# Performance work log

Measured on AMD Instinct MI355X. Metric: run time of the kernel, lower is better.

The kernel has to match this reference:

```python
import jax, jax.numpy as jnp
from jax import lax
import numpy as np

B, C_IN, H, W = 4, 64, 192, 192
NPT = 128          # num_point
MAXC = 32          # objects per image
INIT_STRIDE, COARSE_STRIDE, DOWN = 10.0, 4.0, 4.0


def setup_inputs() -> dict:
    key = jax.random.key(0)
    ks = jax.random.split(key, 8)
    wh_pred = jax.random.normal(ks[0], (B, 2 * NPT, H, W), jnp.float32)
    cnn_feature = jax.random.normal(ks[1], (B, C_IN, H, W), jnp.float32)
    conv1_w = jax.random.normal(ks[2], (256, C_IN, 3, 3), jnp.float32) * 0.05
    conv1_b = jnp.zeros((256,), jnp.float32)
    conv2_w = jax.random.normal(ks[3], (C_IN, 256, 1, 1), jnp.float32) * 0.05
    conv2_b = jnp.zeros((C_IN,), jnp.float32)
    w_poly = jax.random.normal(ks[4], (NPT * 4, (NPT + 1) * C_IN), jnp.float32) * 0.02
    w_fuse = jax.random.normal(ks[5], (NPT * 2, NPT * 4), jnp.float32) * 0.02
    b_fuse = jnp.zeros((NPT * 2,), jnp.float32)
    ct_ind = jax.random.randint(ks[6], (B, MAXC), 0, H * W, jnp.int32)
    ct_img_idx = jnp.repeat(jnp.arange(B, dtype=jnp.int32), MAXC).reshape(B, MAXC)
    ct_num = jnp.full((B,), MAXC, jnp.int32)
    return {"wh_pred": wh_pred, "cnn_feature": cnn_feature,
            "conv1_w": conv1_w, "conv1_b": conv1_b, "conv2_w": conv2_w, "conv2_b": conv2_b,
            "w_poly": w_poly, "w_fuse": w_fuse, "b_fuse": b_fuse,
            "ct_ind": ct_ind, "ct_img_idx": ct_img_idx, "ct_num": ct_num}


def _conv(x, w, b, pad):
    y = lax.conv_general_dilated(x, w, (1, 1), [(pad, pad), (pad, pad)],
                                 dimension_numbers=("NCHW", "OIHW", "NCHW"))
    return y + b[None, :, None, None]


def _pnp(polys, h, w):
    # even-odd ray-casting rasterization: polys [N,P,2] (x,y) -> masks [N,h,w]
    N, P, _ = polys.shape
    yy = jnp.arange(h, dtype=polys.dtype)[None, :, None]   # [1,h,1]
    xx = jnp.arange(w, dtype=polys.dtype)[None, None, :]   # [1,1,w]
    v2 = jnp.roll(polys, -1, axis=1)
    edges = (polys[:, :, 0].T, polys[:, :, 1].T, v2[:, :, 0].T, v2[:, :, 1].T)  # each [P,N]

    def step(par, e):
        x1, y1, x2, y2 = [a[:, None, None] for a in e]      # [N,1,1]
        cond = (y1 > yy) != (y2 > yy)
        den = y2 - y1
        den = jnp.where(jnp.abs(den) < 1e-9, 1e-9, den)
        xint = x1 + (x2 - x1) * (yy - y1) / den
        return jnp.logical_xor(par, cond & (xx < xint)), None

    par0 = jnp.zeros((N, h, w), dtype=bool)
    par, _ = lax.scan(step, par0, edges)
    return par.astype(polys.dtype)


def _mask_batch(mask, ct_num, bs, h, w):
    # faithful to original buggy scatter: offset uses ct_num[i-1], not a cumulative sum
    cn = [int(v) for v in np.asarray(ct_num)]
    mc = max(cn)
    mb = jnp.zeros((bs, mc, h, w), mask.dtype)
    mb = mb.at[0, :cn[0]].set(mask[:cn[0]])
    for i in range(1, bs):
        mb = mb.at[i, :cn[i]].set(mask[cn[i - 1]:cn[i - 1] + cn[i]])
    return mb


def _sample(feat, pts, img_idx):
    # bilinear grid_sample (align_corners=False, zero padding): feat [B,C,H,W], pts [N,P,2] pixel coords
    Bf, C, Hf, Wf = feat.shape
    x = pts[..., 0] - 0.5
    y = pts[..., 1] - 0.5
    x0f = jnp.floor(x); y0f = jnp.floor(y)
    wx = (x - x0f)[..., None]; wy = (y - y0f)[..., None]
    x0 = x0f.astype(jnp.int32); y0 = y0f.astype(jnp.int32)

    def g(xi, yi):
        valid = (xi >= 0) & (xi < Wf) & (yi >= 0) & (yi < Hf)
        v = feat[img_idx[:, None], :, jnp.clip(yi, 0, Hf - 1), jnp.clip(xi, 0, Wf - 1)]  # [N,P,C]
        return v * valid[..., None]

    out = (g(x0, y0) * (1 - wx) * (1 - wy) + g(x0 + 1, y0) * wx * (1 - wy)
           + g(x0, y0 + 1) * (1 - wx) * wy + g(x0 + 1, y0 + 1) * wx * wy)
    return jnp.transpose(out, (0, 2, 1))  # [N,C,P]


def _decode(wh_pred, cnn_feature, conv1_w, conv1_b, conv2_w, conv2_b,
            w_poly, w_fuse, b_fuse, ct_ind, ct_img_idx, ct_num):
    bs, _, h, w = cnn_feature.shape
    ind = ct_ind.reshape(-1)        # ct_01 assumed all valid
    img = ct_img_idx.reshape(-1)
    cx = ind % w
    cy = ind // w
    off = wh_pred[img, :, cy, cx].reshape(ind.shape[0], -1, 2)   # [N, num_point, 2]
    ct = jnp.stack([cx, cy], axis=1).astype(wh_pred.dtype)       # [N,2]
    init_polys = off * INIT_STRIDE + ct[:, None, :]

    # Refine_wtih_pnp.trans_feature
    t = jax.nn.relu(_conv(cnn_feature, conv1_w, conv1_b, 1))
    feat = _conv(t, conv2_w, conv2_b, 0)

    # PnP_contour_feature (init)
    m_init = _pnp(init_polys, h, w)
    mb_init = _mask_batch(m_init, ct_num, bs, h, w)
    feat = jax.nn.relu(jnp.max(mb_init, axis=1, keepdims=True) * feat + feat)

    # GCN-style point feature sampling + global deform
    pts = jnp.concatenate([ct[:, None, :], init_polys], axis=1)  # [N, P+1, 2]
    fp = _sample(feat, pts, img).reshape(ind.shape[0], -1)       # [N, C*(P+1)]
    offsets = ((fp @ w_poly.T) @ w_fuse.T + b_fuse).reshape(-1, NPT, 2)
    coarse = offsets * COARSE_STRIDE + lax.stop_gradient(init_polys)

    # coarse_pnp
    m_c = _pnp(coarse, h, w)
    mb_c = _mask_batch(m_c, ct_num, bs, h, w)
    feat = jax.nn.relu(jnp.max(mb_c, axis=1, keepdims=True) * feat + feat)

    return init_polys * DOWN, coarse * DOWN, mb_init, mb_c, feat


def reference(wh_pred, cnn_feature, conv1_w, conv1_b, conv2_w, conv2_b,
              w_poly, w_fuse, b_fuse, ct_ind, ct_img_idx, ct_num):
    return _decode(wh_pred, cnn_feature, conv1_w, conv1_b, conv2_w, conv2_b,
                   w_poly, w_fuse, b_fuse, ct_ind, ct_img_idx, ct_num)
```

## Files before the change

### kernel.cpp

```cpp
#include <hip/hip_runtime.h>
#include <hip/hip_bf16.h>

#define HH 192
#define WW 192
#define HW 36864
#define CHW 2359296

typedef __attribute__((ext_vector_type(8))) short short8;
typedef __attribute__((ext_vector_type(4))) float float4v;

static __device__ __forceinline__ unsigned short f2bu(float f) {
  union { float f; unsigned u; } v; v.f = f;
  unsigned r = (v.u + 0x7fffu + ((v.u >> 16) & 1u)) >> 16;
  return (unsigned short)r;
}

static __device__ __forceinline__ float bu2f(unsigned short s) {
  union { unsigned u; float f; } v; v.u = ((unsigned)s) << 16;
  return v.f;
}

__global__ void k_prep(const float* __restrict__ c1w, const float* __restrict__ c2w,
                       const float* __restrict__ wfuse,
                       unsigned short* __restrict__ wB1, unsigned short* __restrict__ wB2,
                       float* __restrict__ wfT, float* __restrict__ tmp,
                       float* __restrict__ u01) {
  int i = blockIdx.x * 256 + threadIdx.x;
  if (i < 147456) {
    int T = i / 9216, r = i % 9216;
    int s = r / 512, e = r % 512;
    int l = e >> 3, j = e & 7;
    int m = l & 15, q = l >> 4;
    int oc = T * 16 + m;
    int k = s * 32 + q * 8 + j;
    int tap = k >> 6, ic = k & 63;
    int ky = tap / 3, kx = tap % 3;
    wB1[i] = f2bu(c1w[((oc * 64 + ic) * 3 + ky) * 3 + kx]);
    return;
  }
  int j2 = i - 147456;
  if (j2 < 16384) {
    int g = j2 / 512, e = j2 % 512;
    int l = e >> 3, jj = e & 7;
    int m = l & 15, q = l >> 4;
    int w = g / 8, s2 = g % 8;
    wB2[j2] = f2bu(c2w[(w * 16 + m) * 256 + s2 * 32 + q * 8 + jj]);
    return;
  }
  int k3 = j2 - 16384;
  if (k3 < 131072) { int jj = k3 >> 8, r = k3 & 255; wfT[k3] = wfuse[r * 512 + jj]; return; }
  int z = k3 - 131072;
  if (z < 65536) { tmp[z] = 0.f; return; }
  int v = z - 65536;
  if (v < 294912) u01[v] = 0.f;
}

__global__ void k_init_polys(const float* __restrict__ wh, const int* __restrict__ ct_ind,
                             const int* __restrict__ ct_img,
                             float* __restrict__ initp, float* __restrict__ out0) {
  int n = blockIdx.x;
  int p = threadIdx.x;
  int ind = ct_ind[n], img = ct_img[n];
  int cx = ind % WW, cy = ind / WW;
  size_t base = ((size_t)(img * 256 + 2 * p)) * HW + (size_t)cy * WW + cx;
  float ox = wh[base];
  float oy = wh[base + HW];
  float px = __fadd_rn(__fmul_rn(ox, 10.0f), (float)cx);
  float py = __fadd_rn(__fmul_rn(oy, 10.0f), (float)cy);
  initp[n * 256 + 2 * p]     = px;
  initp[n * 256 + 2 * p + 1] = py;
  out0[n * 256 + 2 * p]      = __fmul_rn(px, 4.0f);
  out0[n * 256 + 2 * p + 1]  = __fmul_rn(py, 4.0f);
}

__global__ __launch_bounds__(256, 3) void k_conv(const float* __restrict__ x,
    const unsigned short* __restrict__ wB1, const float* __restrict__ b1,
    const unsigned short* __restrict__ wB2, const float* __restrict__ b2,
    const float* __restrict__ u0, float* __restrict__ feat,
    unsigned short* __restrict__ featT) {
  int blk = blockIdx.x;
  int b    = blk / 576;
  int rem  = blk % 576;
  int pair = rem / 6;
  int xs   = rem % 6;
  int y0 = pair * 2, x0 = xs * 32;
  int t = threadIdx.x;
  int w = t >> 6, l = t & 63;
  int m = l & 15, q = l >> 4;

  __shared__ __align__(16) unsigned short sb[16896];

  {
    int kq = t & 7;
    int pr = t >> 3;
    for (int itr = 0; itr < 8; ++itr) {
      int pi = itr * 32 + pr;
      int r  = pi >> 6;
      int ic = pi & 63;
      int gy = y0 + r - 1;
      float4v v = (float4v){0.f, 0.f, 0.f, 0.f};
      if (gy >= 0 && gy < HH)
        v = *(const float4v*)&x[(size_t)(b * 64 + ic) * HW + (size_t)gy * WW + x0 + kq * 4];
      int base = (r * 34 + 1 + kq * 4) * 72 + ic;
      sb[base]       = f2bu(v[0]);
      sb[base + 72]  = f2bu(v[1]);
      sb[base + 144] = f2bu(v[2]);
      sb[base + 216] = f2bu(v[3]);
    }
    for (int itr = 0; itr < 2; ++itr) {
      int e = itr * 256 + t;
      int xxh = e >> 8;
      int rm = e & 255;
      int r = rm >> 6, ic = rm & 63;
      int gy = y0 + r - 1;
      int gx = x0 - 1 + xxh * 33;
      float v = 0.f;
      if (gy >= 0 && gy < HH && gx >= 0 && gx < WW)
        v = x[(size_t)(b * 64 + ic) * HW + (size_t)gy * WW + gx];
      sb[(r * 34 + xxh * 33) * 72 + ic] = f2bu(v);
    }
  }
  __syncthreads();

  float4v acc1[4][4];
#pragma unroll
  for (int nt = 0; nt < 4; ++nt) {
    float bv = b1[w * 64 + nt * 16 + m];
#pragma unroll
    for (int mt = 0; mt < 4; ++mt) acc1[mt][nt] = (float4v){bv, bv, bv, bv};
  }

#pragma unroll
  for (int s = 0; s < 18; ++s) {
    int tap = s >> 1, ky = tap / 3, kx = tap - ky * 3;
    int ic0 = (s & 1) * 32 + q * 8;
    short8 bF[4];
#pragma unroll
    for (int nt = 0; nt < 4; ++nt)
      bF[nt] = *(const short8*)&wB1[(size_t)((((w * 4 + nt) * 18 + s) * 512) + l * 8)];
    short8 aF[4];
#pragma unroll
    for (int mt = 0; mt < 4; ++mt) {
      int col  = (mt & 1) * 16 + m + kx;
      int rowi = ky + (mt >> 1);
      aF[mt] = *(const short8*)&sb[(rowi * 34 + col) * 72 + ic0];
    }
#pragma unroll
    for (int nt = 0; nt < 4; ++nt)
#pragma unroll
      for (int mt = 0; mt < 4; ++mt)
        acc1[mt][nt] = __builtin_amdgcn_mfma_f32_16x16x32_bf16(aF[mt], bF[nt], acc1[mt][nt], 0, 0, 0);
  }
  __syncthreads();

#pragma unroll
  for (int mt = 0; mt < 4; ++mt)
#pragma unroll
    for (int nt = 0; nt < 4; ++nt)
#pragma unroll
      for (int r = 0; r < 4; ++r) {
        int p = mt * 16 + q * 4 + r;
        int oc = w * 64 + nt * 16 + m;
        sb[p * 264 + oc] = f2bu(fmaxf(acc1[mt][nt][r], 0.f));
      }
  __syncthreads();

  float4v acc2[4];
  {
    float bv = b2[w * 16 + m];
#pragma unroll
    for (int mt = 0; mt < 4; ++mt) acc2[mt] = (float4v){bv, bv, bv, bv};
  }
#pragma unroll
  for (int s2 = 0; s2 < 8; ++s2) {
    short8 bF2 = *(const short8*)&wB2[(size_t)(((w * 8 + s2) * 512) + l * 8)];
#pragma unroll
    for (int mt = 0; mt < 4; ++mt) {
      short8 a2 = *(const short8*)&sb[(mt * 16 + m) * 264 + s2 * 32 + q * 8];
      acc2[mt] = __builtin_amdgcn_mfma_f32_16x16x32_bf16(a2, bF2, acc2[mt], 0, 0, 0);
    }
  }
  __syncthreads();

  float* fS = (float*)sb;
#pragma unroll
  for (int mt = 0; mt < 4; ++mt)
#pragma unroll
    for (int r = 0; r < 4; ++r) {
      int p = mt * 16 + q * 4 + r;
      fS[w * 1088 + m * 68 + p] = acc2[mt][r];
    }
  const float* ub = u0 + b * HW;
  {
    int gy = y0 + (l >> 5), gx = x0 + (l & 31);
    float uu = ub[gy * WW + gx];
    size_t fb = (size_t)(b * 64 + w * 16) * HW + (size_t)gy * WW + gx;
#pragma unroll
    for (int i = 0; i < 16; ++i) {
      float f = fS[w * 1088 + i * 68 + l];
      feat[fb + (size_t)i * HW] = fmaxf(uu * f + f, 0.f);
    }
  }
  {
    unsigned short* ft = featT + (size_t)b * HW * 64;
    int c2 = (l & 7) * 2;
#pragma unroll
    for (int i = 0; i < 8; ++i) {
      int p = (l >> 3) + 8 * i;
      float f0 = fS[w * 1088 + c2 * 68 + p];
      float f1 = fS[w * 1088 + (c2 + 1) * 68 + p];
      int gy = y0 + (p >> 5), gx = x0 + (p & 31);
      float uu = ub[gy * WW + gx];
      f0 = fmaxf(uu * f0 + f0, 0.f);
      f1 = fmaxf(uu * f1 + f1, 0.f);
      unsigned v = (unsigned)f2bu(f0) | ((unsigned)f2bu(f1) << 16);
      *(unsigned*)&ft[((size_t)(gy * WW + gx)) * 64 + w * 16 + c2] = v;
    }
  }
}

__global__ __launch_bounds__(64) void k_pnp(const float* __restrict__ polys,
                                            float* __restrict__ outm,
                                            float* __restrict__ u) {
  int row  = blockIdx.x;
  int n    = blockIdx.y;
  int lane = threadIdx.x;
  __shared__ float vx[128], vy[128], xint[128];
  __shared__ int cnt;
  if (lane == 0) cnt = 0;
  vx[lane]      = polys[n * 256 + 2 * lane];
  vy[lane]      = polys[n * 256 + 2 * lane + 1];
  vx[lane + 64] = polys[n * 256 + 2 * (lane + 64)];
  vy[lane + 64] = polys[n * 256 + 2 * (lane + 64) + 1];
  __syncthreads();
  float yy = (float)row;
  for (int e = lane; e < 128; e += 64) {
    float y1 = vy[e], y2 = vy[(e + 1) & 127];
    if ((y1 > yy) != (y2 > yy)) {
      float x1 = vx[e], x2 = vx[(e + 1) & 127];
      float den = __fsub_rn(y2, y1);
      if (fabsf(den) < 1e-9f) den = 1e-9f;
      float xi = __fadd_rn(x1, __fdiv_rn(__fmul_rn(__fsub_rn(x2, x1), __fsub_rn(yy, y1)), den));
      xint[atomicAdd(&cnt, 1)] = xi;
    }
  }
  __syncthreads();
  int mm = cnt;
  int bb = (n < 32) ? 0 : 1;
  int cc = n & 31;
  size_t base = ((size_t)(bb * 32 + cc) * HH + row) * WW;
  for (int xp = lane; xp < WW; xp += 64) {
    float xf = (float)xp;
    int c = 0;
    for (int j = 0; j < mm; ++j) c += (xf < xint[j]) ? 1 : 0;
    float mv = (float)(c & 1);
    outm[base + xp] = mv;
    if (n >= 32) {
      outm[base + (size_t)32 * HW + xp] = mv;
      outm[base + (size_t)64 * HW + xp] = mv;
    }
    if (c & 1) {
      int off = bb * HW + row * WW + xp;
      atomicOr((int*)(u + off), 0x3f800000);
      if (n >= 32) {
        atomicOr((int*)(u + off + HW), 0x3f800000);
        atomicOr((int*)(u + off + 2 * HW), 0x3f800000);
      }
    }
  }
}

__global__ __launch_bounds__(256) void k_sample(const unsigned short* __restrict__ featT,
    const float* __restrict__ initp, const int* __restrict__ ct_ind,
    const int* __restrict__ ct_img, float* __restrict__ fp) {
  int n  = blockIdx.x;
  int ch = blockIdx.y;
  int t  = threadIdx.x;
  int w  = t >> 6, lane = t & 63;
  int c  = lane & 31;
  int ph = lane >> 5;

  __shared__ float sF[4128];

  int img = ct_img[n];
  int ind = ct_ind[n];
  float ctx = (float)(ind % WW), cty = (float)(ind / WW);
  const unsigned short* fb = featT + (size_t)img * HW * 64 + ch * 32 + c;

  for (int i = 0; i < 17; ++i) {
    int p = i * 8 + w * 2 + ph;
    if (p < 129) {
      float px, py;
      if (p == 0) { px = ctx; py = cty; }
      else {
        px = initp[n * 256 + 2 * (p - 1)];
        py = initp[n * 256 + 2 * (p - 1) + 1];
      }
      float x = __fsub_rn(px, 0.5f), y = __fsub_rn(py, 0.5f);
      float x0f = floorf(x), y0f = floorf(y);
      float wx = __fsub_rn(x, x0f), wy = __fsub_rn(y, y0f);
      int x0 = (int)x0f, y0 = (int)y0f;
      float g[4];
#pragma unroll
      for (int qq = 0; qq < 4; ++qq) {
        int xi = x0 + (qq & 1), yi = y0 + (qq >> 1);
        bool valid = (xi >= 0) && (xi < WW) && (yi >= 0) && (yi < HH);
        int xc = min(max(xi, 0), WW - 1), yc = min(max(yi, 0), HH - 1);
        float v = bu2f(fb[(size_t)(yc * WW + xc) * 64]);
        g[qq] = valid ? v : 0.f;
      }
      float omx = __fsub_rn(1.f, wx), omy = __fsub_rn(1.f, wy);
      float r = __fadd_rn(__fadd_rn(__fadd_rn(
          __fmul_rn(__fmul_rn(g[0], omx), omy),
          __fmul_rn(__fmul_rn(g[1], wx),  omy)),
          __fmul_rn(__fmul_rn(g[2], omx), wy)),
          __fmul_rn(__fmul_rn(g[3], wx),  wy));
      sF[c * 129 + p] = r;
    }
  }
  __syncthreads();
  float* dst = fp + (size_t)n * 8256 + (size_t)ch * 4128;
  for (int idx = t; idx < 4128; idx += 256) dst[idx] = sF[idx];
}

__global__ __launch_bounds__(256) void k_gemm1(const float* __restrict__ fp,
    const float* __restrict__ wpoly, float* __restrict__ tmp) {
  int ntile = blockIdx.x;
  int jtile = blockIdx.y;
  int ks    = blockIdx.z;
  int c0 = (129 * ks) / 32, c1 = (129 * (ks + 1)) / 32;
  int t = threadIdx.x;
  int tn = t & 15, tj = t >> 4;
  __shared__ float aS[64][65];
  __shared__ float bS[64][65];
  float acc[4][4];
#pragma unroll
  for (int i = 0; i < 4; ++i)
#pragma unroll
    for (int j = 0; j < 4; ++j) acc[i][j] = 0.f;
  for (int ch = c0; ch < c1; ++ch) {
    int k0 = ch * 64;
    __syncthreads();
    for (int idx = t; idx < 4096; idx += 256) {
      int r = idx >> 6, cc = idx & 63;
      aS[cc][r] = fp[(size_t)(ntile * 64 + r) * 8256 + k0 + cc];
      bS[cc][r] = wpoly[(size_t)(jtile * 64 + r) * 8256 + k0 + cc];
    }
    __syncthreads();
    for (int kk = 0; kk < 64; ++kk) {
      float a0 = aS[kk][tn * 4], a1 = aS[kk][tn * 4 + 1], a2 = aS[kk][tn * 4 + 2], a3 = aS[kk][tn * 4 + 3];
      float b0 = bS[kk][tj * 4], b1 = bS[kk][tj * 4 + 1], b2 = bS[kk][tj * 4 + 2], b3 = bS[kk][tj * 4 + 3];
      acc[0][0] = fmaf(a0, b0, acc[0][0]); acc[0][1] = fmaf(a0, b1, acc[0][1]);
      acc[0][2] = fmaf(a0, b2, acc[0][2]); acc[0][3] = fmaf(a0, b3, acc[0][3]);
      acc[1][0] = fmaf(a1, b0, acc[1][0]); acc[1][1] = fmaf(a1, b1, acc[1][1]);
      acc[1][2] = fmaf(a1, b2, acc[1][2]); acc[1][3] = fmaf(a1, b3, acc[1][3]);
      acc[2][0] = fmaf(a2, b0, acc[2][0]); acc[2][1] = fmaf(a2, b1, acc[2][1]);
      acc[2][2] = fmaf(a2, b2, acc[2][2]); acc[2][3] = fmaf(a2, b3, acc[2][3]);
      acc[3][0] = fmaf(a3, b0, acc[3][0]); acc[3][1] = fmaf(a3, b1, acc[3][1]);
      acc[3][2] = fmaf(a3, b2, acc[3][2]); acc[3][3] = fmaf(a3, b3, acc[3][3]);
    }
  }
#pragma unroll
  for (int i = 0; i < 4; ++i)
#pragma unroll
    for (int j = 0; j < 4; ++j)
      atomicAdd(&tmp[(size_t)(ntile * 64 + tn * 4 + i) * 512 + jtile * 64 + tj * 4 + j], acc[i][j]);
}

__global__ __launch_bounds__(256) void k_gemm2(const float* __restrict__ tmp,
    const float* __restrict__ wfT, const float* __restrict__ bfuse,
    const float* __restrict__ initp, float* __restrict__ coarse, float* __restrict__ out1) {
  int n = blockIdx.x, r = threadIdx.x;
  __shared__ float tS[512];
  tS[r] = tmp[n * 512 + r];
  tS[r + 256] = tmp[n * 512 + 256 + r];
  __syncthreads();
  float acc = 0.f;
  for (int j = 0; j < 512; ++j) acc = fmaf(wfT[j * 256 + r], tS[j], acc);
  acc = __fadd_rn(acc, bfuse[r]);
  float cr = __fadd_rn(__fmul_rn(acc, 4.0f), initp[n * 256 + r]);
  coarse[n * 256 + r] = cr;
  out1[n * 256 + r] = __fmul_rn(cr, 4.0f);
}

__global__ void k_final(float* __restrict__ feat, const float* __restrict__ u) {
  size_t i = ((size_t)blockIdx.x * 256 + threadIdx.x) * 4;
  int b = (int)(i / ((size_t)CHW));
  int yx = (int)(i % HW);
  float4v f = *(float4v*)&feat[i];
  float4v uu = *(const float4v*)&u[b * HW + yx];
  float4v o;
#pragma unroll
  for (int j = 0; j < 4; ++j) o[j] = fmaxf(__fadd_rn(__fmul_rn(uu[j], f[j]), f[j]), 0.f);
  *(float4v*)&feat[i] = o;
}

extern "C" void kernel_launch(void* const* d_in, const int* in_sizes, int n_in,
                              void* d_out, int out_size, void* d_ws, size_t ws_size,
                              hipStream_t stream) {
  const float* wh    = (const float*)d_in[0];
  const float* cnnf  = (const float*)d_in[1];
  const float* c1w   = (const float*)d_in[2];
  const float* c1b   = (const float*)d_in[3];
  const float* c2w   = (const float*)d_in[4];
  const float* c2b   = (const float*)d_in[5];
  const float* wpoly = (const float*)d_in[6];
  const float* wfuse = (const float*)d_in[7];
  const float* bfuse = (const float*)d_in[8];
  const int* ct_ind  = (const int*)d_in[9];
  const int* ct_img  = (const int*)d_in[10];

  float* ws    = (float*)d_ws;
  float* wfT   = ws;
  float* initp = wfT + 131072;
  float* coarse= initp + 32768;
  float* tmp   = coarse + 32768;
  float* u0    = tmp + 65536;
  float* u1    = u0 + 147456;
  float* fpbuf = u1 + 147456;
  unsigned short* wB1 = (unsigned short*)(fpbuf + 1056768);
  unsigned short* wB2 = wB1 + 147456;

  float* out0 = (float*)d_out;
  float* out1 = out0 + 32768;
  float* out2 = out1 + 32768;
  float* out3 = out2 + 4718592;
  float* out4 = out3 + 4718592;
  float* feat = out4;
  unsigned short* featT = (unsigned short*)out3;

  k_prep<<<2560, 256, 0, stream>>>(c1w, c2w, wfuse, wB1, wB2, wfT, tmp, u0);
  k_init_polys<<<128, 128, 0, stream>>>(wh, ct_ind, ct_img, initp, out0);
  k_pnp<<<dim3(192, 64), 64, 0, stream>>>(initp, out2, u0);
  k_conv<<<2304, 256, 0, stream>>>(cnnf, wB1, c1b, wB2, c2b, u0, feat, featT);
  k_sample<<<dim3(128, 2), 256, 0, stream>>>(featT, initp, ct_ind, ct_img, fpbuf);
  k_gemm1<<<dim3(2, 8, 32), 256, 0, stream>>>(fpbuf, wpoly, tmp);
  k_gemm2<<<128, 256, 0, stream>>>(tmp, wfT, bfuse, initp, coarse, out1);
  k_pnp<<<dim3(192, 64), 64, 0, stream>>>(coarse, out3, u1);
  k_final<<<9216, 256, 0, stream>>>(feat, u1);
}
```

Baseline: 423.7 us.

## Restructure PnP per image-row, fuse feature gating, vectorize gemm1 loads

The polygon rasterizer now runs one 256-thread block per (row, image). It handles all 32 objects of that image, builds the per-row max mask in shared memory, and writes it directly. This replaces the global atomicOr accumulation and the zero-initialisation of the mask buffers. The second PnP pass also applies the relu(u*f+f) gating to the feature map in place, which removes the separate k_final kernel. gemm1 now loads tiles with float4 reads and reads shared memory as float4. The cost is fewer, heavier blocks that each do serial per-object intersection work.

```diff
diff --git a/kernel.cpp b/kernel.cpp
--- a/kernel.cpp
+++ b/kernel.cpp
@@ -23,8 +23,7 @@
 __global__ void k_prep(const float* __restrict__ c1w, const float* __restrict__ c2w,
                        const float* __restrict__ wfuse,
                        unsigned short* __restrict__ wB1, unsigned short* __restrict__ wB2,
-                       float* __restrict__ wfT, float* __restrict__ tmp,
-                       float* __restrict__ u01) {
+                       float* __restrict__ wfT, float* __restrict__ tmp) {
   int i = blockIdx.x * 256 + threadIdx.x;
   if (i < 147456) {
     int T = i / 9216, r = i % 9216;
@@ -50,9 +49,7 @@
   int k3 = j2 - 16384;
   if (k3 < 131072) { int jj = k3 >> 8, r = k3 & 255; wfT[k3] = wfuse[r * 512 + jj]; return; }
   int z = k3 - 131072;
-  if (z < 65536) { tmp[z] = 0.f; return; }
-  int v = z - 65536;
-  if (v < 294912) u01[v] = 0.f;
+  if (z < 65536) tmp[z] = 0.f;
 }
 
 __global__ void k_init_polys(const float* __restrict__ wh, const int* __restrict__ ct_ind,
@@ -73,6 +70,69 @@
   out0[n * 256 + 2 * p + 1]  = __fmul_rn(py, 4.0f);
 }
 
+__global__ __launch_bounds__(256) void k_pnp(const float* __restrict__ polys,
+    float* __restrict__ outm, float* __restrict__ uout, float* __restrict__ fgate) {
+  int row = blockIdx.x;
+  int b   = blockIdx.y;
+  int t = threadIdx.x;
+  int w = t >> 6, lane = t & 63;
+  __shared__ float xint[32][128];
+  __shared__ int   cnt[32];
+  __shared__ float mrow[32][192];
+  __shared__ float urow[192];
+  if (t < 32) cnt[t] = 0;
+  __syncthreads();
+  int nbase = (b == 0) ? 0 : 32;
+  float yy = (float)row;
+  for (int pc = 0; pc < 8; ++pc) {
+    int c = w * 8 + pc;
+    const float* P = polys + (nbase + c) * 256;
+    for (int e = lane; e < 128; e += 64) {
+      float y1 = P[2 * e + 1], y2 = P[2 * ((e + 1) & 127) + 1];
+      if ((y1 > yy) != (y2 > yy)) {
+        float x1 = P[2 * e], x2 = P[2 * ((e + 1) & 127)];
+        float den = __fsub_rn(y2, y1);
+        if (fabsf(den) < 1e-9f) den = 1e-9f;
+        float xi = __fadd_rn(x1, __fdiv_rn(__fmul_rn(__fsub_rn(x2, x1), __fsub_rn(yy, y1)), den));
+        xint[c][atomicAdd(&cnt[c], 1)] = xi;
+      }
+    }
+  }
+  __syncthreads();
+  for (int idx = t; idx < 32 * 192; idx += 256) {
+    int c = idx / 192, xp = idx - c * 192;
+    float xf = (float)xp;
+    int mm = cnt[c], cr = 0;
+    for (int j = 0; j < mm; ++j) cr += (xf < xint[c][j]) ? 1 : 0;
+    float mv = (float)(cr & 1);
+    mrow[c][xp] = mv;
+    outm[((size_t)(b * 32 + c) * HH + row) * WW + xp] = mv;
+  }
+  __syncthreads();
+  if (t < 192) {
+    float u = 0.f;
+#pragma unroll
+    for (int c = 0; c < 32; ++c) u = fmaxf(u, mrow[c][t]);
+    urow[t] = u;
+    if (uout) uout[(size_t)b * HW + (size_t)row * WW + t] = u;
+  }
+  __syncthreads();
+  if (fgate) {
+    float* fb = fgate + (size_t)b * CHW + (size_t)row * WW;
+    for (int idx = t; idx < 64 * 48; idx += 256) {
+      int chn = idx / 48, qx = idx - chn * 48;
+      float4v f = *(float4v*)&fb[(size_t)chn * HW + qx * 4];
+      float4v o;
+#pragma unroll
+      for (int j = 0; j < 4; ++j) {
+        float uu = urow[qx * 4 + j];
+        o[j] = fmaxf(__fadd_rn(__fmul_rn(uu, f[j]), f[j]), 0.f);
+      }
+      *(float4v*)&fb[(size_t)chn * HW + qx * 4] = o;
+    }
+  }
+}
+
 __global__ __launch_bounds__(256, 3) void k_conv(const float* __restrict__ x,
     const unsigned short* __restrict__ wB1, const float* __restrict__ b1,
     const unsigned short* __restrict__ wB2, const float* __restrict__ b2,
@@ -219,57 +279,6 @@
   }
 }
 
-__global__ __launch_bounds__(64) void k_pnp(const float* __restrict__ polys,
-                                            float* __restrict__ outm,
-                                            float* __restrict__ u) {
-  int row  = blockIdx.x;
-  int n    = blockIdx.y;
-  int lane = threadIdx.x;
-  __shared__ float vx[128], vy[128], xint[128];
-  __shared__ int cnt;
-  if (lane == 0) cnt = 0;
-  vx[lane]      = polys[n * 256 + 2 * lane];
-  vy[lane]      = polys[n * 256 + 2 * lane + 1];
-  vx[lane + 64] = polys[n * 256 + 2 * (lane + 64)];
-  vy[lane + 64] = polys[n * 256 + 2 * (lane + 64) + 1];
-  __syncthreads();
-  float yy = (float)row;
-  for (int e = lane; e < 128; e += 64) {
-    float y1 = vy[e], y2 = vy[(e + 1) & 127];
-    if ((y1 > yy) != (y2 > yy)) {
-      float x1 = vx[e], x2 = vx[(e + 1) & 127];
-      float den = __fsub_rn(y2, y1);
-      if (fabsf(den) < 1e-9f) den = 1e-9f;
-      float xi = __fadd_rn(x1, __fdiv_rn(__fmul_rn(__fsub_rn(x2, x1), __fsub_rn(yy, y1)), den));
-      xint[atomicAdd(&cnt, 1)] = xi;
-    }
-  }
-  __syncthreads();
-  int mm = cnt;
-  int bb = (n < 32) ? 0 : 1;
-  int cc = n & 31;
-  size_t base = ((size_t)(bb * 32 + cc) * HH + row) * WW;
-  for (int xp = lane; xp < WW; xp += 64) {
-    float xf = (float)xp;
-    int c = 0;
-    for (int j = 0; j < mm; ++j) c += (xf < xint[j]) ? 1 : 0;
-    float mv = (float)(c & 1);
-    outm[base + xp] = mv;
-    if (n >= 32) {
-      outm[base + (size_t)32 * HW + xp] = mv;
-      outm[base + (size_t)64 * HW + xp] = mv;
-    }
-    if (c & 1) {
-      int off = bb * HW + row * WW + xp;
-      atomicOr((int*)(u + off), 0x3f800000);
-      if (n >= 32) {
-        atomicOr((int*)(u + off + HW), 0x3f800000);
-        atomicOr((int*)(u + off + 2 * HW), 0x3f800000);
-      }
-    }
-  }
-}
-
 __global__ __launch_bounds__(256) void k_sample(const unsigned short* __restrict__ featT,
     const float* __restrict__ initp, const int* __restrict__ ct_ind,
     const int* __restrict__ ct_img, float* __restrict__ fp) {
@@ -331,8 +340,8 @@
   int c0 = (129 * ks) / 32, c1 = (129 * (ks + 1)) / 32;
   int t = threadIdx.x;
   int tn = t & 15, tj = t >> 4;
-  __shared__ float aS[64][65];
-  __shared__ float bS[64][65];
+  __shared__ __align__(16) float aS[64][68];
+  __shared__ __align__(16) float bS[64][68];
   float acc[4][4];
 #pragma unroll
   for (int i = 0; i < 4; ++i)
@@ -341,23 +350,25 @@
   for (int ch = c0; ch < c1; ++ch) {
     int k0 = ch * 64;
     __syncthreads();
-    for (int idx = t; idx < 4096; idx += 256) {
-      int r = idx >> 6, cc = idx & 63;
-      aS[cc][r] = fp[(size_t)(ntile * 64 + r) * 8256 + k0 + cc];
-      bS[cc][r] = wpoly[(size_t)(jtile * 64 + r) * 8256 + k0 + cc];
+    for (int idx = t; idx < 1024; idx += 256) {
+      int r = idx >> 4, c4 = (idx & 15) * 4;
+      float4v va = *(const float4v*)&fp[(size_t)(ntile * 64 + r) * 8256 + k0 + c4];
+      float4v vb = *(const float4v*)&wpoly[(size_t)(jtile * 64 + r) * 8256 + k0 + c4];
+#pragma unroll
+      for (int d = 0; d < 4; ++d) { aS[c4 + d][r] = va[d]; bS[c4 + d][r] = vb[d]; }
     }
     __syncthreads();
     for (int kk = 0; kk < 64; ++kk) {
-      float a0 = aS[kk][tn * 4], a1 = aS[kk][tn * 4 + 1], a2 = aS[kk][tn * 4 + 2], a3 = aS[kk][tn * 4 + 3];
-      float b0 = bS[kk][tj * 4], b1 = bS[kk][tj * 4 + 1], b2 = bS[kk][tj * 4 + 2], b3 = bS[kk][tj * 4 + 3];
-      acc[0][0] = fmaf(a0, b0, acc[0][0]); acc[0][1] = fmaf(a0, b1, acc[0][1]);
-      acc[0][2] = fmaf(a0, b2, acc[0][2]); acc[0][3] = fmaf(a0, b3, acc[0][3]);
-      acc[1][0] = fmaf(a1, b0, acc[1][0]); acc[1][1] = fmaf(a1, b1, acc[1][1]);
-      acc[1][2] = fmaf(a1, b2, acc[1][2]); acc[1][3] = fmaf(a1, b3, acc[1][3]);
-      acc[2][0] = fmaf(a2, b0, acc[2][0]); acc[2][1] = fmaf(a2, b1, acc[2][1]);
-      acc[2][2] = fmaf(a2, b2, acc[2][2]); acc[2][3] = fmaf(a2, b3, acc[2][3]);
-      acc[3][0] = fmaf(a3, b0, acc[3][0]); acc[3][1] = fmaf(a3, b1, acc[3][1]);
-      acc[3][2] = fmaf(a3, b2, acc[3][2]); acc[3][3] = fmaf(a3, b3, acc[3][3]);
+      float4v a = *(const float4v*)&aS[kk][tn * 4];
+      float4v bq = *(const float4v*)&bS[kk][tj * 4];
+      acc[0][0] = fmaf(a[0], bq[0], acc[0][0]); acc[0][1] = fmaf(a[0], bq[1], acc[0][1]);
+      acc[0][2] = fmaf(a[0], bq[2], acc[0][2]); acc[0][3] = fmaf(a[0], bq[3], acc[0][3]);
+      acc[1][0] = fmaf(a[1], bq[0], acc[1][0]); acc[1][1] = fmaf(a[1], bq[1], acc[1][1]);
+      acc[1][2] = fmaf(a[1], bq[2], acc[1][2]); acc[1][3] = fmaf(a[1], bq[3], acc[1][3]);
+      acc[2][0] = fmaf(a[2], bq[0], acc[2][0]); acc[2][1] = fmaf(a[2], bq[1], acc[2][1]);
+      acc[2][2] = fmaf(a[2], bq[2], acc[2][2]); acc[2][3] = fmaf(a[2], bq[3], acc[2][3]);
+      acc[3][0] = fmaf(a[3], bq[0], acc[3][0]); acc[3][1] = fmaf(a[3], bq[1], acc[3][1]);
+      acc[3][2] = fmaf(a[3], bq[2], acc[3][2]); acc[3][3] = fmaf(a[3], bq[3], acc[3][3]);
     }
   }
 #pragma unroll
@@ -381,18 +392,6 @@
   float cr = __fadd_rn(__fmul_rn(acc, 4.0f), initp[n * 256 + r]);
   coarse[n * 256 + r] = cr;
   out1[n * 256 + r] = __fmul_rn(cr, 4.0f);
-}
-
-__global__ void k_final(float* __restrict__ feat, const float* __restrict__ u) {
-  size_t i = ((size_t)blockIdx.x * 256 + threadIdx.x) * 4;
-  int b = (int)(i / ((size_t)CHW));
-  int yx = (int)(i % HW);
-  float4v f = *(float4v*)&feat[i];
-  float4v uu = *(const float4v*)&u[b * HW + yx];
-  float4v o;
-#pragma unroll
-  for (int j = 0; j < 4; ++j) o[j] = fmaxf(__fadd_rn(__fmul_rn(uu[j], f[j]), f[j]), 0.f);
-  *(float4v*)&feat[i] = o;
 }
 
 extern "C" void kernel_launch(void* const* d_in, const int* in_sizes, int n_in,
@@ -416,8 +415,7 @@
   float* coarse= initp + 32768;
   float* tmp   = coarse + 32768;
   float* u0    = tmp + 65536;
-  float* u1    = u0 + 147456;
-  float* fpbuf = u1 + 147456;
+  float* fpbuf = u0 + 147456;
   unsigned short* wB1 = (unsigned short*)(fpbuf + 1056768);
   unsigned short* wB2 = wB1 + 147456;
 
@@ -429,13 +427,12 @@
   float* feat = out4;
   unsigned short* featT = (unsigned short*)out3;
 
-  k_prep<<<2560, 256, 0, stream>>>(c1w, c2w, wfuse, wB1, wB2, wfT, tmp, u0);
+  k_prep<<<1408, 256, 0, stream>>>(c1w, c2w, wfuse, wB1, wB2, wfT, tmp);
   k_init_polys<<<128, 128, 0, stream>>>(wh, ct_ind, ct_img, initp, out0);
-  k_pnp<<<dim3(192, 64), 64, 0, stream>>>(initp, out2, u0);
+  k_pnp<<<dim3(192, 4), 256, 0, stream>>>(initp, out2, u0, nullptr);
   k_conv<<<2304, 256, 0, stream>>>(cnnf, wB1, c1b, wB2, c2b, u0, feat, featT);
   k_sample<<<dim3(128, 2), 256, 0, stream>>>(featT, initp, ct_ind, ct_img, fpbuf);
   k_gemm1<<<dim3(2, 8, 32), 256, 0, stream>>>(fpbuf, wpoly, tmp);
   k_gemm2<<<128, 256, 0, stream>>>(tmp, wfT, bfuse, initp, coarse, out1);
-  k_pnp<<<dim3(192, 64), 64, 0, stream>>>(coarse, out3, u1);
-  k_final<<<9216, 256, 0, stream>>>(feat, u1);
-}
+  k_pnp<<<dim3(192, 4), 256, 0, stream>>>(coarse, out3, nullptr, feat);
+}
```

New measurement: 432.3 us. 1.02x slower.
